# Kernel optimization log

Measured on AMD Instinct MI355X. Metric: run time of the kernel, lower is better.

## Reference

```python
import jax, jax.numpy as jnp
import numpy as np

EPS = 1e-12  # torch F.normalize default eps

def _l2norm(x):
    n = jnp.sqrt(jnp.sum(x * x, axis=-1, keepdims=True))
    return x / jnp.maximum(n, EPS)

def setup_inputs() -> dict:
    key = jax.random.key(0)
    k1, k2, k3 = jax.random.split(key, 3)
    N, S, D = 65536, 2048, 512
    return {
        "query": jax.random.normal(k1, (N, D), dtype=jnp.float32),
        "keys": jax.random.normal(k2, (S, D), dtype=jnp.float32),
        "values": jax.random.normal(k3, (S, D), dtype=jnp.float32),
    }

def reference(query, keys, values):
    q = _l2norm(query)            # [N, D]
    k = _l2norm(keys)             # [S, D]
    scores = jnp.einsum('nd,sd->ns', q, k)   # [N, S] cosine scores
    attn = jax.nn.softmax(scores, axis=-1)   # [N, S]
    return jnp.einsum('ns,sd->nd', attn, values)  # [N, D]
```

## Files before the change

### kernel.cpp

```cpp
#include <hip/hip_runtime.h>
#include <hip/hip_bf16.h>

typedef __attribute__((ext_vector_type(8))) short short8;
typedef __attribute__((ext_vector_type(4))) float f32x4;
typedef __attribute__((ext_vector_type(2))) unsigned int u32x2;

constexpr int D_DIM = 512;
constexpr int S_DIM = 2048;

static __device__ __forceinline__ unsigned short f2bf(float f) {
  __hip_bfloat16 h = __float2bfloat16(f);
  return *reinterpret_cast<unsigned short*>(&h);
}

#define GLP(p) ((const __attribute__((address_space(1))) unsigned int*)(p))
#define LDP(p) ((__attribute__((address_space(3))) unsigned int*)(p))

static __device__ __forceinline__ void blockbar() {
  asm volatile("" ::: "memory");
  __builtin_amdgcn_s_barrier();
  asm volatile("" ::: "memory");
}

__global__ void k_norm(const float* __restrict__ K, ushort* __restrict__ Kn) {
  const int row = blockIdx.x * 4 + (threadIdx.x >> 6);
  const int l   = threadIdx.x & 63;
  const float* src = K + (size_t)row * D_DIM + l * 8;
  float4 v0 = *(const float4*)(src);
  float4 v1 = *(const float4*)(src + 4);
  float ss = v0.x*v0.x + v0.y*v0.y + v0.z*v0.z + v0.w*v0.w
           + v1.x*v1.x + v1.y*v1.y + v1.z*v1.z + v1.w*v1.w;
  #pragma unroll
  for (int off = 1; off < 64; off <<= 1) ss += __shfl_xor(ss, off, 64);
  const float sc = 1.0f / fmaxf(sqrtf(ss), 1e-12f);
  float f[8] = {v0.x,v0.y,v0.z,v0.w,v1.x,v1.y,v1.z,v1.w};
  unsigned uu[4];
  #pragma unroll
  for (int i = 0; i < 4; ++i)
    uu[i] = (unsigned)f2bf(f[2*i]*sc) | ((unsigned)f2bf(f[2*i+1]*sc) << 16);
  *(uint4*)(Kn + (size_t)row * D_DIM + l*8) = make_uint4(uu[0],uu[1],uu[2],uu[3]);
}

__global__ void k_transpose_v(const float* __restrict__ V, ushort* __restrict__ Vt) {
  __shared__ float tile[64][65];
  const int s0 = blockIdx.x * 64;
  const int d0 = blockIdx.y * 64;
  const int tj = threadIdx.x & 63;
  const int ti = threadIdx.x >> 6;
  #pragma unroll
  for (int k = 0; k < 16; ++k) {
    int s = ti + 4*k;
    tile[s][tj] = V[(size_t)(s0+s) * D_DIM + d0 + tj];
  }
  __syncthreads();
  #pragma unroll
  for (int k = 0; k < 16; ++k) {
    int d = ti + 4*k;
    Vt[(size_t)(d0+d) * S_DIM + s0 + tj] = f2bf(tile[tj][d]);
  }
}

template <int EPI>
__global__ __launch_bounds__(512, 2) void gemm_bt(
    const ushort* __restrict__ A, const ushort* __restrict__ B,
    int aStride, int bStride,
    int NT,
    ushort* __restrict__ Pout, float* __restrict__ Oout,
    float* __restrict__ rowsum,
    int ldC)
{
  __shared__ ushort lds[2][4][8192];
  char* ldsb = (char*)&lds[0][0][0];

  const int tid = threadIdx.x;
  const int w   = tid >> 6;
  const int l   = tid & 63;
  const int lhi = l >> 4;
  const int llo = l & 15;
  const int wm  = w >> 2;
  const int wn  = w & 3;
  const size_t m0 = (size_t)blockIdx.x * 256;
  const size_t n0 = (size_t)blockIdx.y * 256;

  const char* Ab = (const char*)A;
  const char* Bb = (const char*)B;

  const int srow = tid >> 3;
  const int scb  = (tid & 7) * 16;
  auto stage = [&](int buf, int slot, int t) {
    const char* src; int stride; size_t r0;
    if (slot < 2) { src = Ab; stride = aStride; r0 = m0 + (size_t)slot * 128; }
    else          { src = Bb; stride = bStride; r0 = n0 + (size_t)(slot - 2) * 128; }
    char* lbase = ldsb + ((buf*4 + slot) * 16384) + w * 1024;
    {
      const int row = srow;
      const char* g = src + (r0 + row) * (size_t)stride + t*128 + (scb ^ ((row & 7) << 4));
      __builtin_amdgcn_global_load_lds(GLP(g), LDP(lbase), 16, 0, 0);
    }
    {
      const int row = srow + 64;
      const char* g = src + (r0 + row) * (size_t)stride + t*128 + (scb ^ ((row & 7) << 4));
      __builtin_amdgcn_global_load_lds(GLP(g), LDP(lbase + 8192), 16, 0, 0);
    }
  };

  const unsigned swz = (unsigned)((l & 7) << 4);
  short8 ar[4][2], br01[2][2], br23[2][2];
  f32x4 acc[8][4] = {};

  const char* aBase0 = ldsb + wm * 16384;
  const char* bBase0 = ldsb + (2 + (wn >> 1)) * 16384;
  const unsigned bRow0 = (unsigned)((wn & 1) * 64);

  auto readA = [&](int buf, int rfB) {
    const char* base = aBase0 + buf * 65536;
    #pragma unroll
    for (int rf = 0; rf < 4; ++rf)
      #pragma unroll
      for (int kk = 0; kk < 2; ++kk) {
        unsigned off = (unsigned)(((rfB + rf) * 16 + llo) * 128)
                     + (((unsigned)(kk*64 + lhi*16)) ^ swz);
        ar[rf][kk] = *(const short8*)(base + off);
      }
  };
  auto readB = [&](int buf, int cfB, short8 (&br)[2][2]) {
    const char* base = bBase0 + buf * 65536;
    #pragma unroll
    for (int c = 0; c < 2; ++c)
      #pragma unroll
      for (int kk = 0; kk < 2; ++kk) {
        unsigned off = (unsigned)((bRow0 + (cfB + c) * 16 + llo) * 128)
                     + (((unsigned)(kk*64 + lhi*16)) ^ swz);
        br[c][kk] = *(const short8*)(base + off);
      }
  };
  auto quad = [&](int rfB, int cfB, short8 (&br)[2][2]) {
    __builtin_amdgcn_s_setprio(1);
    #pragma unroll
    for (int kk = 0; kk < 2; ++kk)
      #pragma unroll
      for (int rf = 0; rf < 4; ++rf)
        #pragma unroll
        for (int c = 0; c < 2; ++c)
          acc[rfB+rf][cfB+c] = __builtin_amdgcn_mfma_f32_16x16x32_bf16(
              ar[rf][kk], br[c][kk], acc[rfB+rf][cfB+c], 0, 0, 0);
    __builtin_amdgcn_s_setprio(0);
  };

  stage(0, 2, 0); stage(0, 0, 0); stage(0, 1, 0); stage(0, 3, 0);
  stage(1, 2, 1); stage(1, 0, 1);

  for (int t = 0; t < NT; ++t) {
    const int cur = t & 1, nxt = cur ^ 1;
    if (t + 1 < NT) asm volatile("s_waitcnt vmcnt(4)" ::: "memory");
    else            asm volatile("s_waitcnt vmcnt(0)" ::: "memory");
    blockbar();
    readA(cur, 0);
    readB(cur, 0, br01);
    if (t + 1 < NT) stage(nxt, 1, t + 1);
    quad(0, 0, br01);
    blockbar();
    readB(cur, 2, br23);
    if (t + 1 < NT) stage(nxt, 3, t + 1);
    quad(0, 2, br23);
    blockbar();
    readA(cur, 4);
    if (t + 2 < NT) stage(cur, 2, t + 2);
    quad(4, 2, br23);
    blockbar();
    if (t + 2 < NT) stage(cur, 0, t + 2);
    quad(4, 0, br01);
  }

  if (EPI == 0) {
    #pragma unroll
    for (int rf = 0; rf < 8; ++rf) {
      float e[4][4];
      #pragma unroll
      for (int cf = 0; cf < 4; ++cf)
        #pragma unroll
        for (int j = 0; j < 4; ++j)
          e[cf][j] = __expf(acc[rf][cf][j]);
      #pragma unroll
      for (int j = 0; j < 4; ++j) {
        const size_t m = m0 + wm*128 + rf*16 + lhi*4 + j;
        #pragma unroll
        for (int cf = 0; cf < 4; ++cf) {
          const size_t n = n0 + wn*64 + cf*16 + llo;
          Pout[m * (size_t)ldC + n] = f2bf(e[cf][j]);
        }
        float rp = (e[0][j] + e[1][j]) + (e[2][j] + e[3][j]);
        rp += __shfl_xor(rp, 1, 64);
        rp += __shfl_xor(rp, 2, 64);
        rp += __shfl_xor(rp, 4, 64);
        rp += __shfl_xor(rp, 8, 64);
        if (llo == 0) atomicAdd(&rowsum[m], rp);
      }
    }
  } else {
    #pragma unroll
    for (int rf = 0; rf < 8; ++rf)
      #pragma unroll
      for (int j = 0; j < 4; ++j) {
        const size_t m = m0 + wm*128 + rf*16 + lhi*4 + j;
        const float inv = 1.0f / rowsum[m];
        #pragma unroll
        for (int cf = 0; cf < 4; ++cf) {
          const size_t n = n0 + wn*64 + cf*16 + llo;
          Oout[m * (size_t)ldC + n] = acc[rf][cf][j] * inv;
        }
      }
  }
}

constexpr int BMf = 64, BHf = 256, NHf = S_DIM / BHf, NWf = 8;
constexpr int PBUFf = BMf * BHf * 2;

__global__ __launch_bounds__(512, 2) void attn_fused(
    const float* __restrict__ Q, const ushort* __restrict__ Kn,
    const ushort* __restrict__ Vt, float* __restrict__ out)
{
  __shared__ ushort q_s[BMf * D_DIM];
  __shared__ ushort p_s[2 * BMf * BHf];
  __shared__ float  rs_lds[NWf * BMf];
  __shared__ float  rs_tot[BMf];
  char* qb = (char*)q_s;
  char* pb = (char*)p_s;
  const int tid = threadIdx.x;
  const int w   = tid >> 6;
  const int l   = tid & 63;
  const int lhi = l >> 4;
  const int llo = l & 15;
  const size_t q0 = (size_t)blockIdx.x * BMf;
  {
    const int row = tid >> 3;
    const int c   = tid & 7;
    const unsigned swzr = (unsigned)((row & 7) << 4);
    const float4* src = (const float4*)(Q + (q0 + row) * D_DIM);
    float4 t[16];
    float ss = 0.f;
    #pragma unroll
    for (int i = 0; i < 16; ++i) {
      t[i] = src[c + i*8];
      ss += t[i].x*t[i].x + t[i].y*t[i].y + t[i].z*t[i].z + t[i].w*t[i].w;
    }
    ss += __shfl_xor(ss, 1, 64);
    ss += __shfl_xor(ss, 2, 64);
    ss += __shfl_xor(ss, 4, 64);
    const float sc = 1.0f / fmaxf(sqrtf(ss), 1e-12f);
    #pragma unroll
    for (int i = 0; i < 16; ++i) {
      u32x2 pv;
      pv[0] = (unsigned)f2bf(t[i].x*sc) | ((unsigned)f2bf(t[i].y*sc) << 16);
      pv[1] = (unsigned)f2bf(t[i].z*sc) | ((unsigned)f2bf(t[i].w*sc) << 16);
      unsigned byte = (unsigned)(row*1024) + (((unsigned)(c*8 + i*64)) ^ swzr);
      *(u32x2*)(qb + byte) = pv;
    }
  }
  __syncthreads();
  f32x4 o[4][4] = {};
  float rs_acc[4] = {0.f, 0.f, 0.f, 0.f};
  const unsigned swz = (unsigned)((l & 7) << 4);
  unsigned rowbQ[4], rowbP[4];
  #pragma unroll
  for (int qf = 0; qf < 4; ++qf) {
    rowbQ[qf] = (unsigned)((qf*16 + llo) * 1024);
    rowbP[qf] = (unsigned)((qf*16 + llo) * 512);
  }
  auto do_qkt = [&](int h, f32x4 (&sacc)[2][4]) {
    const short8* kp[2];
    #pragma unroll
    for (int kf = 0; kf < 2; ++kf)
      kp[kf] = (const short8*)(Kn + (size_t)(h*BHf + w*32 + kf*16 + llo) * D_DIM + lhi*8);
    __builtin_amdgcn_s_setprio(1);
    #pragma unroll
    for (int ks = 0; ks < 16; ++ks) {
      const unsigned off = ((unsigned)(ks*64 + lhi*16)) ^ swz;
      short8 a[2], b[4];
      #pragma unroll
      for (int kf = 0; kf < 2; ++kf) a[kf] = kp[kf][ks*4];
      #pragma unroll
      for (int qf = 0; qf < 4; ++qf)
        b[qf] = *(const short8*)(qb + (rowbQ[qf] + off));
      #pragma unroll
      for (int kf = 0; kf < 2; ++kf)
        #pragma unroll
        for (int qf = 0; qf < 4; ++qf)
          sacc[kf][qf] = __builtin_amdgcn_mfma_f32_16x16x32_bf16(a[kf], b[qf], sacc[kf][qf], 0, 0, 0);
    }
    __builtin_amdgcn_s_setprio(0);
  };
  auto do_exp = [&](f32x4 (&sacc)[2][4], u32x2 (&pk)[2][4]) {
    #pragma unroll
    for (int kf = 0; kf < 2; ++kf)
      #pragma unroll
      for (int qf = 0; qf < 4; ++qf) {
        float p0 = __expf(sacc[kf][qf][0]);
        float p1 = __expf(sacc[kf][qf][1]);
        float p2 = __expf(sacc[kf][qf][2]);
        float p3 = __expf(sacc[kf][qf][3]);
        rs_acc[qf] += (p0 + p1) + (p2 + p3);
        pk[kf][qf][0] = (unsigned)f2bf(p0) | ((unsigned)f2bf(p1) << 16);
        pk[kf][qf][1] = (unsigned)f2bf(p2) | ((unsigned)f2bf(p3) << 16);
      }
  };
  auto do_pwrite = [&](u32x2 (&pk)[2][4], char* buf) {
    #pragma unroll
    for (int kf = 0; kf < 2; ++kf)
      #pragma unroll
      for (int qf = 0; qf < 4; ++qf) {
        unsigned lin = (unsigned)(w*64 + kf*32 + lhi*8);
        *(u32x2*)(buf + rowbP[qf] + (lin ^ swz)) = pk[kf][qf];
      }
  };
  auto do_pv = [&](int h, const char* buf) {
    const short8* vp[4];
    #pragma unroll
    for (int df = 0; df < 4; ++df)
      vp[df] = (const short8*)(Vt + (size_t)(w*64 + df*16 + llo) * S_DIM + h*BHf + lhi*8);
    __builtin_amdgcn_s_setprio(1);
    #pragma unroll
    for (int ks = 0; ks < 8; ++ks) {
      const unsigned off = ((unsigned)(ks*64 + lhi*16)) ^ swz;
      short8 a[4], b[4];
      #pragma unroll
      for (int qf = 0; qf < 4; ++qf)
        a[qf] = *(const short8*)(buf + (rowbP[qf] + off));
      #pragma unroll
      for (int df = 0; df < 4; ++df) b[df] = vp[df][ks*4];
      #pragma unroll
      for (int qf = 0; qf < 4; ++qf)
        #pragma unroll
        for (int df = 0; df < 4; ++df)
          o[qf][df] = __builtin_amdgcn_mfma_f32_16x16x32_bf16(a[qf], b[df], o[qf][df], 0, 0, 0);
    }
    __builtin_amdgcn_s_setprio(0);
  };
  {
    f32x4 sacc[2][4] = {};
    do_qkt(0, sacc);
    u32x2 pk[2][4];
    do_exp(sacc, pk);
    do_pwrite(pk, pb + 0);
  }
  __syncthreads();
  for (int i = 0; i < NHf - 1; ++i) {
    f32x4 sacc[2][4] = {};
    do_qkt(i + 1, sacc);
    u32x2 pk[2][4];
    do_exp(sacc, pk);
    do_pv(i, pb + (i & 1) * PBUFf);
    do_pwrite(pk, pb + ((i + 1) & 1) * PBUFf);
    __syncthreads();
  }
  do_pv(NHf - 1, pb + ((NHf - 1) & 1) * PBUFf);
  #pragma unroll
  for (int qf = 0; qf < 4; ++qf) {
    float v = rs_acc[qf];
    v += __shfl_xor(v, 16, 64);
    v += __shfl_xor(v, 32, 64);
    if (l < 16) rs_lds[w*BMf + qf*16 + llo] = v;
  }
  __syncthreads();
  if (tid < BMf) {
    float tot = 0.f;
    #pragma unroll
    for (int ww = 0; ww < NWf; ++ww) tot += rs_lds[ww*BMf + tid];
    rs_tot[tid] = tot;
  }
  __syncthreads();
  #pragma unroll
  for (int qf = 0; qf < 4; ++qf)
    #pragma unroll
    for (int r = 0; r < 4; ++r) {
      const int query = qf*16 + lhi*4 + r;
      const float inv = 1.0f / rs_tot[query];
      #pragma unroll
      for (int df = 0; df < 4; ++df) {
        const int dim = w*64 + df*16 + llo;
        out[(q0 + query) * D_DIM + dim] = o[qf][df][r] * inv;
      }
    }
}

extern "C" void kernel_launch(void* const* d_in, const int* in_sizes, int n_in,
                              void* d_out, int out_size, void* d_ws, size_t ws_size,
                              hipStream_t stream) {
  const float* Q = (const float*)d_in[0];
  const float* K = (const float*)d_in[1];
  const float* V = (const float*)d_in[2];
  float* out = (float*)d_out;
  const int N = in_sizes[0] / D_DIM;

  ushort* Kn = (ushort*)d_ws;
  ushort* Vt = Kn + (size_t)S_DIM * D_DIM;
  char*   rest = (char*)(Vt + (size_t)D_DIM * S_DIM);
  const size_t base_bytes = (size_t)S_DIM * D_DIM * 2 * 2;
  const size_t avail = ws_size > base_bytes ? ws_size - base_bytes : 0;

  const size_t perRow = (size_t)D_DIM*2 + (size_t)S_DIM*2 + 4;
  int chunk = 0;
  const int cand[4] = {32768, 16384, 8192, 4096};
  for (int i = 0; i < 4; ++i)
    if ((size_t)cand[i] * perRow <= avail && (N % cand[i]) == 0) { chunk = cand[i]; break; }

  k_norm<<<S_DIM/4, 256, 0, stream>>>(K, Kn);
  k_transpose_v<<<dim3(S_DIM/64, D_DIM/64), 256, 0, stream>>>(V, Vt);

  if (chunk == 0) {
    attn_fused<<<N/BMf, 512, 0, stream>>>(Q, Kn, Vt, out);
    return;
  }

  ushort* Qn = (ushort*)rest;
  ushort* P  = Qn + (size_t)chunk * D_DIM;
  float* rowsum = (float*)(P + (size_t)chunk * S_DIM);

  for (int c = 0; c < N; c += chunk) {
    k_norm<<<chunk/4, 256, 0, stream>>>(Q + (size_t)c * D_DIM, Qn);
    hipMemsetAsync(rowsum, 0, (size_t)chunk * 4, stream);
    gemm_bt<0><<<dim3(chunk/256, S_DIM/256), 512, 0, stream>>>(
        Qn, Kn, D_DIM*2, D_DIM*2, D_DIM/64, P, nullptr, rowsum, S_DIM);
    gemm_bt<1><<<dim3(chunk/256, D_DIM/256), 512, 0, stream>>>(
        P, Vt, S_DIM*2, S_DIM*2, S_DIM/64, nullptr,
        out + (size_t)c * D_DIM, rowsum, D_DIM);
  }
}
```

Before: 359.7 us.

## Split GEMM into two kernels with smaller M tile and triple buffering for P·V

The templated GEMM becomes two kernels. The P·V GEMM now uses 128x256 tiles with a three-stage LDS ring, which doubles the number of blocks for the narrow D=512 output to improve occupancy and latency hiding. Both kernels also remap block IDs so neighbouring tiles land on the same XCD for L2 locality. The cost is lower per-block reuse of the Vt tile and more total B loads.

```diff
diff --git a/kernel.cpp b/kernel.cpp
--- a/kernel.cpp
+++ b/kernel.cpp
@@ -20,6 +20,17 @@
   asm volatile("" ::: "memory");
   __builtin_amdgcn_s_barrier();
   asm volatile("" ::: "memory");
+}
+
+static __device__ __forceinline__ void xcd_remap(int gx, int gy, int& bx, int& by) {
+  const int nwg = gx * gy;
+  int lin = by * gx + bx;
+  if ((nwg & 7) == 0) {
+    const int cpx = nwg >> 3;
+    lin = (lin & 7) * cpx + (lin >> 3);
+  }
+  bx = lin % gx;
+  by = lin / gx;
 }
 
 __global__ void k_norm(const float* __restrict__ K, ushort* __restrict__ Kn) {
@@ -60,13 +71,11 @@
   }
 }
 
-template <int EPI>
-__global__ __launch_bounds__(512, 2) void gemm_bt(
+__global__ __launch_bounds__(512, 2) void gemm1_bt(
     const ushort* __restrict__ A, const ushort* __restrict__ B,
     int aStride, int bStride,
     int NT,
-    ushort* __restrict__ Pout, float* __restrict__ Oout,
-    float* __restrict__ rowsum,
+    ushort* __restrict__ Pout, float* __restrict__ rowsum,
     int ldC)
 {
   __shared__ ushort lds[2][4][8192];
@@ -79,8 +88,10 @@
   const int llo = l & 15;
   const int wm  = w >> 2;
   const int wn  = w & 3;
-  const size_t m0 = (size_t)blockIdx.x * 256;
-  const size_t n0 = (size_t)blockIdx.y * 256;
+  int bx = blockIdx.x, by = blockIdx.y;
+  xcd_remap(gridDim.x, gridDim.y, bx, by);
+  const size_t m0 = (size_t)bx * 256;
+  const size_t n0 = (size_t)by * 256;
 
   const char* Ab = (const char*)A;
   const char* Bb = (const char*)B;
@@ -172,45 +183,149 @@
     quad(4, 0, br01);
   }
 
-  if (EPI == 0) {
-    #pragma unroll
-    for (int rf = 0; rf < 8; ++rf) {
-      float e[4][4];
-      #pragma unroll
-      for (int cf = 0; cf < 4; ++cf)
+  #pragma unroll
+  for (int rf = 0; rf < 8; ++rf) {
+    float e[4][4];
+    #pragma unroll
+    for (int cf = 0; cf < 4; ++cf)
+      #pragma unroll
+      for (int j = 0; j < 4; ++j)
+        e[cf][j] = __expf(acc[rf][cf][j]);
+    #pragma unroll
+    for (int j = 0; j < 4; ++j) {
+      const size_t m = m0 + wm*128 + rf*16 + lhi*4 + j;
+      #pragma unroll
+      for (int cf = 0; cf < 4; ++cf) {
+        const size_t n = n0 + wn*64 + cf*16 + llo;
+        Pout[m * (size_t)ldC + n] = f2bf(e[cf][j]);
+      }
+      float rp = (e[0][j] + e[1][j]) + (e[2][j] + e[3][j]);
+      rp += __shfl_xor(rp, 1, 64);
+      rp += __shfl_xor(rp, 2, 64);
+      rp += __shfl_xor(rp, 4, 64);
+      rp += __shfl_xor(rp, 8, 64);
+      if (llo == 0) atomicAdd(&rowsum[m], rp);
+    }
+  }
+}
+
+__global__ __launch_bounds__(512, 2) void gemm2_bt(
+    const ushort* __restrict__ A, const ushort* __restrict__ B,
+    int aStride, int bStride,
+    int NT,
+    float* __restrict__ Oout, const float* __restrict__ rowsum,
+    int ldC)
+{
+  __shared__ ushort lds[3][3][8192];
+  char* ldsb = (char*)&lds[0][0][0];
+
+  const int tid = threadIdx.x;
+  const int w   = tid >> 6;
+  const int l   = tid & 63;
+  const int lhi = l >> 4;
+  const int llo = l & 15;
+  const int wm  = w >> 2;
+  const int wn  = w & 3;
+  int bx = blockIdx.x, by = blockIdx.y;
+  xcd_remap(gridDim.x, gridDim.y, bx, by);
+  const size_t m0 = (size_t)bx * 128;
+  const size_t n0 = (size_t)by * 256;
+
+  const char* Ab = (const char*)A;
+  const char* Bb = (const char*)B;
+
+  const int srow = tid >> 3;
+  const int scb  = (tid & 7) * 16;
+  auto stage = [&](int buf, int slot, int t) {
+    const char* src; int stride; size_t r0;
+    if (slot == 0) { src = Ab; stride = aStride; r0 = m0; }
+    else           { src = Bb; stride = bStride; r0 = n0 + (size_t)(slot - 1) * 128; }
+    char* lbase = ldsb + ((buf*3 + slot) * 16384) + w * 1024;
+    {
+      const int row = srow;
+      const char* g = src + (r0 + row) * (size_t)stride + t*128 + (scb ^ ((row & 7) << 4));
+      __builtin_amdgcn_global_load_lds(GLP(g), LDP(lbase), 16, 0, 0);
+    }
+    {
+      const int row = srow + 64;
+      const char* g = src + (r0 + row) * (size_t)stride + t*128 + (scb ^ ((row & 7) << 4));
+      __builtin_amdgcn_global_load_lds(GLP(g), LDP(lbase + 8192), 16, 0, 0);
+    }
+  };
+
+  const unsigned swz = (unsigned)((l & 7) << 4);
+  short8 ar[4][2], br01[2][2], br23[2][2];
+  f32x4 acc[4][4] = {};
+
+  const unsigned aRow0 = (unsigned)(wm * 64);
+  const int bSlot = 1 + (wn >> 1);
+  const unsigned bRow0 = (unsigned)((wn & 1) * 64);
+
+  auto readA = [&](int buf) {
+    const char* base = ldsb + (buf*3) * 16384;
+    #pragma unroll
+    for (int rf = 0; rf < 4; ++rf)
+      #pragma unroll
+      for (int kk = 0; kk < 2; ++kk) {
+        unsigned off = (unsigned)((aRow0 + rf*16 + llo) * 128)
+                     + (((unsigned)(kk*64 + lhi*16)) ^ swz);
+        ar[rf][kk] = *(const short8*)(base + off);
+      }
+  };
+  auto readB = [&](int buf, int cfB, short8 (&br)[2][2]) {
+    const char* base = ldsb + (buf*3 + bSlot) * 16384;
+    #pragma unroll
+    for (int c = 0; c < 2; ++c)
+      #pragma unroll
+      for (int kk = 0; kk < 2; ++kk) {
+        unsigned off = (unsigned)((bRow0 + (cfB + c) * 16 + llo) * 128)
+                     + (((unsigned)(kk*64 + lhi*16)) ^ swz);
+        br[c][kk] = *(const short8*)(base + off);
+      }
+  };
+  auto quad = [&](int cfB, short8 (&br)[2][2]) {
+    __builtin_amdgcn_s_setprio(1);
+    #pragma unroll
+    for (int kk = 0; kk < 2; ++kk)
+      #pragma unroll
+      for (int rf = 0; rf < 4; ++rf)
         #pragma unroll
-        for (int j = 0; j < 4; ++j)
-          e[cf][j] = __expf(acc[rf][cf][j]);
-      #pragma unroll
-      for (int j = 0; j < 4; ++j) {
-        const size_t m = m0 + wm*128 + rf*16 + lhi*4 + j;
-        #pragma unroll
-        for (int cf = 0; cf < 4; ++cf) {
-          const size_t n = n0 + wn*64 + cf*16 + llo;
-          Pout[m * (size_t)ldC + n] = f2bf(e[cf][j]);
-        }
-        float rp = (e[0][j] + e[1][j]) + (e[2][j] + e[3][j]);
-        rp += __shfl_xor(rp, 1, 64);
-        rp += __shfl_xor(rp, 2, 64);
-        rp += __shfl_xor(rp, 4, 64);
-        rp += __shfl_xor(rp, 8, 64);
-        if (llo == 0) atomicAdd(&rowsum[m], rp);
-      }
-    }
-  } else {
-    #pragma unroll
-    for (int rf = 0; rf < 8; ++rf)
-      #pragma unroll
-      for (int j = 0; j < 4; ++j) {
-        const size_t m = m0 + wm*128 + rf*16 + lhi*4 + j;
-        const float inv = 1.0f / rowsum[m];
-        #pragma unroll
-        for (int cf = 0; cf < 4; ++cf) {
-          const size_t n = n0 + wn*64 + cf*16 + llo;
-          Oout[m * (size_t)ldC + n] = acc[rf][cf][j] * inv;
-        }
-      }
-  }
+        for (int c = 0; c < 2; ++c)
+          acc[rf][cfB+c] = __builtin_amdgcn_mfma_f32_16x16x32_bf16(
+              ar[rf][kk], br[c][kk], acc[rf][cfB+c], 0, 0, 0);
+    __builtin_amdgcn_s_setprio(0);
+  };
+
+  stage(0, 0, 0); stage(0, 1, 0); stage(0, 2, 0);
+  stage(1, 0, 1); stage(1, 1, 1); stage(1, 2, 1);
+
+  for (int t = 0; t < NT; ++t) {
+    const int cur = t % 3, nx2 = (t + 2) % 3;
+    if (t + 1 < NT) asm volatile("s_waitcnt vmcnt(6)" ::: "memory");
+    else            asm volatile("s_waitcnt vmcnt(0)" ::: "memory");
+    blockbar();
+    readA(cur);
+    readB(cur, 0, br01);
+    if (t + 2 < NT) { stage(nx2, 0, t + 2); stage(nx2, 1, t + 2); }
+    quad(0, br01);
+    blockbar();
+    readB(cur, 2, br23);
+    if (t + 2 < NT) stage(nx2, 2, t + 2);
+    quad(2, br23);
+  }
+
+  #pragma unroll
+  for (int rf = 0; rf < 4; ++rf)
+    #pragma unroll
+    for (int j = 0; j < 4; ++j) {
+      const size_t m = m0 + wm*64 + rf*16 + lhi*4 + j;
+      const float inv = 1.0f / rowsum[m];
+      #pragma unroll
+      for (int cf = 0; cf < 4; ++cf) {
+        const size_t n = n0 + wn*64 + cf*16 + llo;
+        Oout[m * (size_t)ldC + n] = acc[rf][cf][j] * inv;
+      }
+    }
 }
 
 constexpr int BMf = 64, BHf = 256, NHf = S_DIM / BHf, NWf = 8;
@@ -419,10 +534,10 @@
   for (int c = 0; c < N; c += chunk) {
     k_norm<<<chunk/4, 256, 0, stream>>>(Q + (size_t)c * D_DIM, Qn);
     hipMemsetAsync(rowsum, 0, (size_t)chunk * 4, stream);
-    gemm_bt<0><<<dim3(chunk/256, S_DIM/256), 512, 0, stream>>>(
-        Qn, Kn, D_DIM*2, D_DIM*2, D_DIM/64, P, nullptr, rowsum, S_DIM);
-    gemm_bt<1><<<dim3(chunk/256, D_DIM/256), 512, 0, stream>>>(
-        P, Vt, S_DIM*2, S_DIM*2, S_DIM/64, nullptr,
+    gemm1_bt<<<dim3(chunk/256, S_DIM/256), 512, 0, stream>>>(
+        Qn, Kn, D_DIM*2, D_DIM*2, D_DIM/64, P, rowsum, S_DIM);
+    gemm2_bt<<<dim3(chunk/128, D_DIM/256), 512, 0, stream>>>(
+        P, Vt, S_DIM*2, S_DIM*2, S_DIM/64,
         out + (size_t)c * D_DIM, rowsum, D_DIM);
   }
 }
```

Measured after the change: 395.2 us. 1.1x slower.
